# Kernel optimization log

Hardware: AMD Instinct MI355X
Metric: run time of the kernel (lower is better)

The kernel has to match this reference:

```python
import jax, jax.numpy as jnp
import numpy as np


def setup_inputs() -> dict:
    key = jax.random.key(0)
    ks = jax.random.split(key, 6)
    T, O, D = 1024, 512, 256
    H = 2 * D
    s = 1.0 / np.sqrt(H)
    return {
        "z_t": jax.random.normal(ks[0], (T, D), jnp.float32),
        "z_o": jax.random.normal(ks[1], (O, D), jnp.float32),
        "W1": jax.random.normal(ks[2], (H, H), jnp.float32) * s,
        "b1": jax.random.normal(ks[3], (H,), jnp.float32) * s,
        "W2": jax.random.normal(ks[4], (H, 1), jnp.float32) * s,
        "b2": jax.random.normal(ks[5], (1,), jnp.float32) * s,
    }


def reference(z_t, z_o, W1, b1, W2, b2):
    # Original: cat([z_t expand, z_o expand], -1) @ W1 + b1 -> LeakyReLU -> @ W2 + b2
    # Decompose the concat GEMM: [z_t | z_o] @ W1 == z_t @ W1[:D] + z_o @ W1[D:]
    D = z_t.shape[-1]
    ht = z_t @ W1[:D]              # [T, 2D]
    ho = z_o @ W1[D:]              # [O, 2D]
    h = ht[:, None, :] + ho[None, :, :] + b1   # [T, O, 2D]
    h = jax.nn.leaky_relu(h, negative_slope=0.01)
    out = jnp.squeeze(h @ W2, -1) + b2[0]      # [T, O]
    return out
```

## Files before the change

### kernel.cpp

```cpp
#include <hip/hip_runtime.h>
#include <cstdint>

#define T_DIM 1024
#define O_DIM 512
#define D_DIM 256
#define H_DIM 512
#define H2_DIM 256

typedef _Float16 f16x2 __attribute__((ext_vector_type(2)));
typedef _Float16 f16x8 __attribute__((ext_vector_type(8)));
typedef float f32x4 __attribute__((ext_vector_type(4)));

__device__ __forceinline__ uint32_t pack2(float a, float b) {
    f16x2 p;
    p.x = (_Float16)a;
    p.y = (_Float16)b;
    return __builtin_bit_cast(uint32_t, p);
}

__device__ __forceinline__ uint32_t pk_add(uint32_t a, uint32_t b) {
    uint32_t d;
    asm("v_pk_add_f16 %0, %1, %2" : "=v"(d) : "v"(a), "v"(b));
    return d;
}
__device__ __forceinline__ uint32_t pk_mul(uint32_t a, uint32_t b) {
    uint32_t d;
    asm("v_pk_mul_f16 %0, %1, %2" : "=v"(d) : "v"(a), "v"(b));
    return d;
}
__device__ __forceinline__ uint32_t pk_max(uint32_t a, uint32_t b) {
    uint32_t d;
    asm("v_pk_max_f16 %0, %1, %2" : "=v"(d) : "v"(a), "v"(b));
    return d;
}
__device__ __forceinline__ float dot2(uint32_t a, uint32_t b, float c) {
    float d;
    asm("v_dot2_f32_f16 %0, %1, %2, %3" : "=v"(d) : "v"(a), "v"(b), "v"(c));
    return d;
}

struct u4 { uint32_t x, y, z, w; };

#define GA_PAD 20

__global__ __launch_bounds__(256) void gemm_a(
    const float* __restrict__ z_t, const float* __restrict__ z_o,
    const float* __restrict__ W1, const float* __restrict__ b1,
    uint32_t* __restrict__ htT2, uint32_t* __restrict__ hoT2)
{
    const int bm = blockIdx.x;
    const int bn = blockIdx.y;
    const bool is_o = bm >= (T_DIM / 64);
    const float* Amat = is_o ? z_o : z_t;
    const int m0 = (is_o ? bm - T_DIM / 64 : bm) * 64;
    const int n0 = bn * 64;
    const int krow0 = is_o ? D_DIM : 0;
    const int Mdim = is_o ? O_DIM : T_DIM;
    uint32_t* outT2 = is_o ? hoT2 : htT2;

    __shared__ __align__(16) uint32_t lds_a[64 * GA_PAD];
    __shared__ __align__(16) uint32_t lds_w[64 * GA_PAD];

    const int tid = threadIdx.x;
    const int lane = tid & 63;
    const int wv = tid >> 6;
    const int quad = lane >> 4;
    const int l15 = lane & 15;

    f32x4 acc[4];
#pragma unroll
    for (int i = 0; i < 4; ++i) acc[i] = (f32x4)(0.0f);

    const int a_m = tid >> 2;
    const int a_kq = (tid & 3) * 8;
    const int w_kp = tid >> 4;
    const int w_nq = (tid & 15) * 4;

    for (int k0 = 0; k0 < D_DIM; k0 += 32) {
        {
            const float* p = &Amat[(size_t)(m0 + a_m) * D_DIM + k0 + a_kq];
            float4 v0 = *reinterpret_cast<const float4*>(p);
            float4 v1 = *reinterpret_cast<const float4*>(p + 4);
            lds_a[a_m * GA_PAD + a_kq / 2 + 0] = pack2(v0.x, v0.y);
            lds_a[a_m * GA_PAD + a_kq / 2 + 1] = pack2(v0.z, v0.w);
            lds_a[a_m * GA_PAD + a_kq / 2 + 2] = pack2(v1.x, v1.y);
            lds_a[a_m * GA_PAD + a_kq / 2 + 3] = pack2(v1.z, v1.w);
        }
        {
            const float* r0 = &W1[(size_t)(krow0 + k0 + 2 * w_kp) * H_DIM + n0 + w_nq];
            float4 a0 = *reinterpret_cast<const float4*>(r0);
            float4 a1 = *reinterpret_cast<const float4*>(r0 + H_DIM);
            lds_w[(w_nq + 0) * GA_PAD + w_kp] = pack2(a0.x, a1.x);
            lds_w[(w_nq + 1) * GA_PAD + w_kp] = pack2(a0.y, a1.y);
            lds_w[(w_nq + 2) * GA_PAD + w_kp] = pack2(a0.z, a1.z);
            lds_w[(w_nq + 3) * GA_PAD + w_kp] = pack2(a0.w, a1.w);
        }
        __syncthreads();

        u4 au;
        {
            const uint32_t* s = &lds_w[(wv * 16 + l15) * GA_PAD + quad * 4];
            au.x = s[0]; au.y = s[1]; au.z = s[2]; au.w = s[3];
        }
        f16x8 afrag = __builtin_bit_cast(f16x8, au);
#pragma unroll
        for (int mi = 0; mi < 4; ++mi) {
            u4 bu;
            const uint32_t* s = &lds_a[(mi * 16 + l15) * GA_PAD + quad * 4];
            bu.x = s[0]; bu.y = s[1]; bu.z = s[2]; bu.w = s[3];
            f16x8 bfrag = __builtin_bit_cast(f16x8, bu);
            acc[mi] = __builtin_amdgcn_mfma_f32_16x16x32_f16(afrag, bfrag,
                                                             acc[mi], 0, 0, 0);
        }
        __syncthreads();
    }

    const int nbase = n0 + wv * 16 + quad * 4;
    float b0 = 0.f, b1v = 0.f, b2v = 0.f, b3v = 0.f;
    if (!is_o) {
        b0 = b1[nbase + 0]; b1v = b1[nbase + 1];
        b2v = b1[nbase + 2]; b3v = b1[nbase + 3];
    }
#pragma unroll
    for (int mi = 0; mi < 4; ++mi) {
        const int m = m0 + mi * 16 + l15;
        outT2[(size_t)((nbase >> 1) + 0) * Mdim + m] = pack2(acc[mi][0] + b0, acc[mi][1] + b1v);
        outT2[(size_t)((nbase >> 1) + 1) * Mdim + m] = pack2(acc[mi][2] + b2v, acc[mi][3] + b3v);
    }
}

#define R_HC 64

__global__ __launch_bounds__(256) void reduce_b(
    const uint32_t* __restrict__ htT2, const uint32_t* __restrict__ hoT2,
    const float* __restrict__ W2, float* __restrict__ part)
{
    __shared__ __align__(16) uint32_t ht_s[R_HC * 64];
    __shared__ __align__(16) uint32_t ho_s[R_HC * 64];
    __shared__ uint32_t w2s[R_HC];

    const int tid = threadIdx.x;
    const int t0 = blockIdx.x * 64;
    const int o0 = blockIdx.y * 64;
    const int h2b = blockIdx.z * R_HC;

    if (tid < R_HC)
        w2s[tid] = pack2(W2[(h2b + tid) * 2], W2[(h2b + tid) * 2 + 1]);

#pragma unroll
    for (int r = 0; r < 4; ++r) {
        const int c = tid + r * 256;
        const int row = c >> 4;
        const int c4 = (c & 15) * 4;
        *reinterpret_cast<uint4*>(&ht_s[row * 64 + c4]) =
            *reinterpret_cast<const uint4*>(&htT2[(size_t)(h2b + row) * T_DIM + t0 + c4]);
        *reinterpret_cast<uint4*>(&ho_s[row * 64 + c4]) =
            *reinterpret_cast<const uint4*>(&hoT2[(size_t)(h2b + row) * O_DIM + o0 + c4]);
    }
    __syncthreads();

    const int tx = tid & 15;
    const int ty = tid >> 4;

    const uint32_t c001 = pack2(0.01f, 0.01f);

    float acc[4][4] = {};

#pragma unroll 4
    for (int h2 = 0; h2 < R_HC; ++h2) {
        const uint32_t w = w2s[h2];
        uint4 a = *reinterpret_cast<const uint4*>(&ht_s[h2 * 64 + ty * 4]);
        uint4 b = *reinterpret_cast<const uint4*>(&ho_s[h2 * 64 + tx * 4]);
        uint32_t av[4] = {a.x, a.y, a.z, a.w};
        uint32_t bv[4] = {b.x, b.y, b.z, b.w};
#pragma unroll
        for (int i = 0; i < 4; ++i)
#pragma unroll
            for (int j = 0; j < 4; ++j) {
                uint32_t s  = pk_add(av[i], bv[j]);
                uint32_t s2 = pk_mul(s, c001);
                uint32_t l  = pk_max(s, s2);
                acc[i][j]   = dot2(l, w, acc[i][j]);
            }
    }

    float* p = part + (size_t)blockIdx.z * T_DIM * O_DIM;
#pragma unroll
    for (int i = 0; i < 4; ++i) {
        float4 v = make_float4(acc[i][0], acc[i][1], acc[i][2], acc[i][3]);
        *reinterpret_cast<float4*>(
            &p[(size_t)(t0 + ty * 4 + i) * O_DIM + o0 + tx * 4]) = v;
    }
}

__global__ __launch_bounds__(256) void combine(
    const float* __restrict__ part, const float* __restrict__ b2,
    float* __restrict__ out)
{
    const float bb = b2[0];
    const int Q = T_DIM * O_DIM / 4;
#pragma unroll
    for (int r = 0; r < 2; ++r) {
        const int idx = blockIdx.x * 512 + r * 256 + threadIdx.x;
        const float4* p = reinterpret_cast<const float4*>(part);
        float4 s0 = p[idx];
        float4 s1 = p[idx + Q];
        float4 s2 = p[idx + 2 * Q];
        float4 s3 = p[idx + 3 * Q];
        float4 o;
        o.x = bb + (s0.x + s1.x) + (s2.x + s3.x);
        o.y = bb + (s0.y + s1.y) + (s2.y + s3.y);
        o.z = bb + (s0.z + s1.z) + (s2.z + s3.z);
        o.w = bb + (s0.w + s1.w) + (s2.w + s3.w);
        reinterpret_cast<float4*>(out)[idx] = o;
    }
}

extern "C" void kernel_launch(void* const* d_in, const int* in_sizes, int n_in,
                              void* d_out, int out_size, void* d_ws, size_t ws_size,
                              hipStream_t stream) {
    const float* z_t = (const float*)d_in[0];
    const float* z_o = (const float*)d_in[1];
    const float* W1  = (const float*)d_in[2];
    const float* b1  = (const float*)d_in[3];
    const float* W2  = (const float*)d_in[4];
    const float* b2  = (const float*)d_in[5];
    float* out = (float*)d_out;

    char* wsb = (char*)d_ws;
    uint32_t* htT2 = (uint32_t*)(wsb);
    uint32_t* hoT2 = (uint32_t*)(wsb + (1u << 20));
    float* part    = (float*)(wsb + 0x200000);

    dim3 gridA((T_DIM + O_DIM) / 64, H_DIM / 64);
    gemm_a<<<gridA, 256, 0, stream>>>(z_t, z_o, W1, b1, htT2, hoT2);

    dim3 gridB(T_DIM / 64, O_DIM / 64, H2_DIM / R_HC);
    reduce_b<<<gridB, 256, 0, stream>>>(htT2, hoT2, W2, part);

    combine<<<T_DIM * O_DIM / (4 * 512), 256, 0, stream>>>(part, b2, out);
}
```

Baseline: 95.54 us.

## Rewrite LeakyReLU as linear plus abs term, enlarge reduce tile, prefetch GEMM loads

The reduce kernel now uses the identity leaky_relu(x) = 0.505x + 0.495|x|. The inner loop computes only the abs term with a sign-bit mask, which replaces the multiply and max per element. The linear part is separable and is computed as per-row and per-column dot products with W2, then added back in combine. The reduce tile grows to 128x64 with 8x4 accumulators per thread and a software-prefetched next h2 row. The GEMM stage register-prefetches the next K slice of global loads so they overlap the MFMA work. The costs are higher register pressure, extra small workspace buffers and more reads in combine.

```diff
diff --git a/kernel.cpp b/kernel.cpp
--- a/kernel.cpp
+++ b/kernel.cpp
@@ -21,16 +21,6 @@
 __device__ __forceinline__ uint32_t pk_add(uint32_t a, uint32_t b) {
     uint32_t d;
     asm("v_pk_add_f16 %0, %1, %2" : "=v"(d) : "v"(a), "v"(b));
-    return d;
-}
-__device__ __forceinline__ uint32_t pk_mul(uint32_t a, uint32_t b) {
-    uint32_t d;
-    asm("v_pk_mul_f16 %0, %1, %2" : "=v"(d) : "v"(a), "v"(b));
-    return d;
-}
-__device__ __forceinline__ uint32_t pk_max(uint32_t a, uint32_t b) {
-    uint32_t d;
-    asm("v_pk_max_f16 %0, %1, %2" : "=v"(d) : "v"(a), "v"(b));
     return d;
 }
 __device__ __forceinline__ float dot2(uint32_t a, uint32_t b, float c) {
@@ -76,26 +66,36 @@
     const int w_kp = tid >> 4;
     const int w_nq = (tid & 15) * 4;
 
+    float4 va0, va1, wa0, wa1;
+    {
+        const float* p = &Amat[(size_t)(m0 + a_m) * D_DIM + a_kq];
+        va0 = *reinterpret_cast<const float4*>(p);
+        va1 = *reinterpret_cast<const float4*>(p + 4);
+        const float* r0 = &W1[(size_t)(krow0 + 2 * w_kp) * H_DIM + n0 + w_nq];
+        wa0 = *reinterpret_cast<const float4*>(r0);
+        wa1 = *reinterpret_cast<const float4*>(r0 + H_DIM);
+    }
+
     for (int k0 = 0; k0 < D_DIM; k0 += 32) {
-        {
-            const float* p = &Amat[(size_t)(m0 + a_m) * D_DIM + k0 + a_kq];
-            float4 v0 = *reinterpret_cast<const float4*>(p);
-            float4 v1 = *reinterpret_cast<const float4*>(p + 4);
-            lds_a[a_m * GA_PAD + a_kq / 2 + 0] = pack2(v0.x, v0.y);
-            lds_a[a_m * GA_PAD + a_kq / 2 + 1] = pack2(v0.z, v0.w);
-            lds_a[a_m * GA_PAD + a_kq / 2 + 2] = pack2(v1.x, v1.y);
-            lds_a[a_m * GA_PAD + a_kq / 2 + 3] = pack2(v1.z, v1.w);
+        lds_a[a_m * GA_PAD + a_kq / 2 + 0] = pack2(va0.x, va0.y);
+        lds_a[a_m * GA_PAD + a_kq / 2 + 1] = pack2(va0.z, va0.w);
+        lds_a[a_m * GA_PAD + a_kq / 2 + 2] = pack2(va1.x, va1.y);
+        lds_a[a_m * GA_PAD + a_kq / 2 + 3] = pack2(va1.z, va1.w);
+        lds_w[(w_nq + 0) * GA_PAD + w_kp] = pack2(wa0.x, wa1.x);
+        lds_w[(w_nq + 1) * GA_PAD + w_kp] = pack2(wa0.y, wa1.y);
+        lds_w[(w_nq + 2) * GA_PAD + w_kp] = pack2(wa0.z, wa1.z);
+        lds_w[(w_nq + 3) * GA_PAD + w_kp] = pack2(wa0.w, wa1.w);
+        __syncthreads();
+
+        if (k0 + 32 < D_DIM) {
+            const float* p = &Amat[(size_t)(m0 + a_m) * D_DIM + k0 + 32 + a_kq];
+            va0 = *reinterpret_cast<const float4*>(p);
+            va1 = *reinterpret_cast<const float4*>(p + 4);
+            const float* r0 =
+                &W1[(size_t)(krow0 + k0 + 32 + 2 * w_kp) * H_DIM + n0 + w_nq];
+            wa0 = *reinterpret_cast<const float4*>(r0);
+            wa1 = *reinterpret_cast<const float4*>(r0 + H_DIM);
         }
-        {
-            const float* r0 = &W1[(size_t)(krow0 + k0 + 2 * w_kp) * H_DIM + n0 + w_nq];
-            float4 a0 = *reinterpret_cast<const float4*>(r0);
-            float4 a1 = *reinterpret_cast<const float4*>(r0 + H_DIM);
-            lds_w[(w_nq + 0) * GA_PAD + w_kp] = pack2(a0.x, a1.x);
-            lds_w[(w_nq + 1) * GA_PAD + w_kp] = pack2(a0.y, a1.y);
-            lds_w[(w_nq + 2) * GA_PAD + w_kp] = pack2(a0.z, a1.z);
-            lds_w[(w_nq + 3) * GA_PAD + w_kp] = pack2(a0.w, a1.w);
-        }
-        __syncthreads();
 
         u4 au;
         {
@@ -129,89 +129,148 @@
     }
 }
 
-#define R_HC 64
+#define RB_T 128
+#define RB_O 64
+#define RB_H2 64
 
 __global__ __launch_bounds__(256) void reduce_b(
     const uint32_t* __restrict__ htT2, const uint32_t* __restrict__ hoT2,
-    const float* __restrict__ W2, float* __restrict__ part)
+    const float* __restrict__ W2, float* __restrict__ part,
+    float* __restrict__ ctp, float* __restrict__ cop)
 {
-    __shared__ __align__(16) uint32_t ht_s[R_HC * 64];
-    __shared__ __align__(16) uint32_t ho_s[R_HC * 64];
-    __shared__ uint32_t w2s[R_HC];
+    __shared__ __align__(16) uint32_t ht_s[RB_H2 * RB_T];
+    __shared__ __align__(16) uint32_t ho_s[RB_H2 * RB_O];
+    __shared__ uint32_t w2s[RB_H2];
+    __shared__ float red_t[2][RB_T];
+    __shared__ float red_o[4][RB_O];
 
     const int tid = threadIdx.x;
-    const int t0 = blockIdx.x * 64;
-    const int o0 = blockIdx.y * 64;
-    const int h2b = blockIdx.z * R_HC;
-
-    if (tid < R_HC)
-        w2s[tid] = pack2(W2[(h2b + tid) * 2], W2[(h2b + tid) * 2 + 1]);
-
+    const int t0 = blockIdx.x * RB_T;
+    const int o0 = blockIdx.y * RB_O;
+    const int h2b = blockIdx.z * RB_H2;
+
+    if (tid < RB_H2)
+        w2s[tid] = pack2(0.495f * W2[(h2b + tid) * 2],
+                         0.495f * W2[(h2b + tid) * 2 + 1]);
+
+#pragma unroll
+    for (int r = 0; r < 8; ++r) {
+        const int c = tid + r * 256;
+        const int row = c >> 5;
+        const int c4 = (c & 31) * 4;
+        *reinterpret_cast<uint4*>(&ht_s[row * RB_T + c4]) =
+            *reinterpret_cast<const uint4*>(
+                &htT2[(size_t)(h2b + row) * T_DIM + t0 + c4]);
+    }
 #pragma unroll
     for (int r = 0; r < 4; ++r) {
         const int c = tid + r * 256;
         const int row = c >> 4;
         const int c4 = (c & 15) * 4;
-        *reinterpret_cast<uint4*>(&ht_s[row * 64 + c4]) =
-            *reinterpret_cast<const uint4*>(&htT2[(size_t)(h2b + row) * T_DIM + t0 + c4]);
-        *reinterpret_cast<uint4*>(&ho_s[row * 64 + c4]) =
-            *reinterpret_cast<const uint4*>(&hoT2[(size_t)(h2b + row) * O_DIM + o0 + c4]);
+        *reinterpret_cast<uint4*>(&ho_s[row * RB_O + c4]) =
+            *reinterpret_cast<const uint4*>(
+                &hoT2[(size_t)(h2b + row) * O_DIM + o0 + c4]);
     }
     __syncthreads();
 
-    const int tx = tid & 15;
-    const int ty = tid >> 4;
-
-    const uint32_t c001 = pack2(0.01f, 0.01f);
-
-    float acc[4][4] = {};
+    const int og = tid & 15;
+    const int tg = tid >> 4;
+
+    float acc[8][4] = {};
+
+    uint4 a0 = *reinterpret_cast<const uint4*>(&ht_s[tg * 8]);
+    uint4 a1 = *reinterpret_cast<const uint4*>(&ht_s[tg * 8 + 4]);
+    uint4 b  = *reinterpret_cast<const uint4*>(&ho_s[og * 4]);
+    uint32_t w = w2s[0];
 
 #pragma unroll 4
-    for (int h2 = 0; h2 < R_HC; ++h2) {
-        const uint32_t w = w2s[h2];
-        uint4 a = *reinterpret_cast<const uint4*>(&ht_s[h2 * 64 + ty * 4]);
-        uint4 b = *reinterpret_cast<const uint4*>(&ho_s[h2 * 64 + tx * 4]);
-        uint32_t av[4] = {a.x, a.y, a.z, a.w};
-        uint32_t bv[4] = {b.x, b.y, b.z, b.w};
-#pragma unroll
-        for (int i = 0; i < 4; ++i)
+    for (int h2 = 0; h2 < RB_H2; ++h2) {
+        const int hn = (h2 + 1) & (RB_H2 - 1);
+        uint4 na0 = *reinterpret_cast<const uint4*>(&ht_s[hn * RB_T + tg * 8]);
+        uint4 na1 = *reinterpret_cast<const uint4*>(&ht_s[hn * RB_T + tg * 8 + 4]);
+        uint4 nb  = *reinterpret_cast<const uint4*>(&ho_s[hn * RB_O + og * 4]);
+        const uint32_t nw = w2s[hn];
+
+        const uint32_t av[8] = {a0.x, a0.y, a0.z, a0.w, a1.x, a1.y, a1.z, a1.w};
+        const uint32_t bv[4] = {b.x, b.y, b.z, b.w};
+#pragma unroll
+        for (int i = 0; i < 8; ++i)
 #pragma unroll
             for (int j = 0; j < 4; ++j) {
-                uint32_t s  = pk_add(av[i], bv[j]);
-                uint32_t s2 = pk_mul(s, c001);
-                uint32_t l  = pk_max(s, s2);
-                acc[i][j]   = dot2(l, w, acc[i][j]);
+                const uint32_t s = pk_add(av[i], bv[j]);
+                const uint32_t l = s & 0x7FFF7FFFu;
+                acc[i][j] = dot2(l, w, acc[i][j]);
             }
+        a0 = na0; a1 = na1; b = nb; w = nw;
     }
 
     float* p = part + (size_t)blockIdx.z * T_DIM * O_DIM;
 #pragma unroll
-    for (int i = 0; i < 4; ++i) {
+    for (int i = 0; i < 8; ++i) {
         float4 v = make_float4(acc[i][0], acc[i][1], acc[i][2], acc[i][3]);
         *reinterpret_cast<float4*>(
-            &p[(size_t)(t0 + ty * 4 + i) * O_DIM + o0 + tx * 4]) = v;
+            &p[(size_t)(t0 + tg * 8 + i) * O_DIM + o0 + og * 4]) = v;
+    }
+
+    {
+        const int t = tid & 127, half = tid >> 7;
+        float s = 0.f;
+#pragma unroll 8
+        for (int j = 0; j < 32; ++j)
+            s = dot2(ht_s[(half * 32 + j) * RB_T + t], w2s[half * 32 + j], s);
+        red_t[half][t] = s;
+        const int o = tid & 63, q = tid >> 6;
+        float so = 0.f;
+#pragma unroll 8
+        for (int j = 0; j < 16; ++j)
+            so = dot2(ho_s[(q * 16 + j) * RB_O + o], w2s[q * 16 + j], so);
+        red_o[q][o] = so;
+    }
+    __syncthreads();
+    if (tid < RB_T) {
+        ctp[(size_t)blockIdx.z * T_DIM + t0 + tid] = red_t[0][tid] + red_t[1][tid];
+    } else if (tid < RB_T + RB_O) {
+        const int o = tid - RB_T;
+        cop[(size_t)blockIdx.z * O_DIM + o0 + o] =
+            red_o[0][o] + red_o[1][o] + red_o[2][o] + red_o[3][o];
     }
 }
 
 __global__ __launch_bounds__(256) void combine(
-    const float* __restrict__ part, const float* __restrict__ b2,
+    const float* __restrict__ part, const float* __restrict__ ctp,
+    const float* __restrict__ cop, const float* __restrict__ b2,
     float* __restrict__ out)
 {
     const float bb = b2[0];
+    const float KLIN = 0.505f / 0.495f;
     const int Q = T_DIM * O_DIM / 4;
+    const float4* cop4 = reinterpret_cast<const float4*>(cop);
+    const float4* p4 = reinterpret_cast<const float4*>(part);
 #pragma unroll
     for (int r = 0; r < 2; ++r) {
         const int idx = blockIdx.x * 512 + r * 256 + threadIdx.x;
-        const float4* p = reinterpret_cast<const float4*>(part);
-        float4 s0 = p[idx];
-        float4 s1 = p[idx + Q];
-        float4 s2 = p[idx + 2 * Q];
-        float4 s3 = p[idx + 3 * Q];
+        const int t = idx >> 7;
+        const int oc = idx & 127;
+        const float ct = ctp[t] + ctp[T_DIM + t] + ctp[2 * T_DIM + t]
+                       + ctp[3 * T_DIM + t];
+        float4 co = cop4[oc];
+        const float4 c1 = cop4[128 + oc];
+        const float4 c2 = cop4[256 + oc];
+        const float4 c3 = cop4[384 + oc];
+        co.x += c1.x + c2.x + c3.x;
+        co.y += c1.y + c2.y + c3.y;
+        co.z += c1.z + c2.z + c3.z;
+        co.w += c1.w + c2.w + c3.w;
+        const float4 s0 = p4[idx];
+        const float4 s1 = p4[idx + Q];
+        const float4 s2 = p4[idx + 2 * Q];
+        const float4 s3 = p4[idx + 3 * Q];
+        const float base = bb + KLIN * ct;
         float4 o;
-        o.x = bb + (s0.x + s1.x) + (s2.x + s3.x);
-        o.y = bb + (s0.y + s1.y) + (s2.y + s3.y);
-        o.z = bb + (s0.z + s1.z) + (s2.z + s3.z);
-        o.w = bb + (s0.w + s1.w) + (s2.w + s3.w);
+        o.x = base + KLIN * co.x + (s0.x + s1.x) + (s2.x + s3.x);
+        o.y = base + KLIN * co.y + (s0.y + s1.y) + (s2.y + s3.y);
+        o.z = base + KLIN * co.z + (s0.z + s1.z) + (s2.z + s3.z);
+        o.w = base + KLIN * co.w + (s0.w + s1.w) + (s2.w + s3.w);
         reinterpret_cast<float4*>(out)[idx] = o;
     }
 }
@@ -229,14 +288,16 @@
 
     char* wsb = (char*)d_ws;
     uint32_t* htT2 = (uint32_t*)(wsb);
-    uint32_t* hoT2 = (uint32_t*)(wsb + (1u << 20));
+    uint32_t* hoT2 = (uint32_t*)(wsb + 0x100000);
+    float* ctp     = (float*)(wsb + 0x180000);
+    float* cop     = (float*)(wsb + 0x184000);
     float* part    = (float*)(wsb + 0x200000);
 
     dim3 gridA((T_DIM + O_DIM) / 64, H_DIM / 64);
     gemm_a<<<gridA, 256, 0, stream>>>(z_t, z_o, W1, b1, htT2, hoT2);
 
-    dim3 gridB(T_DIM / 64, O_DIM / 64, H2_DIM / R_HC);
-    reduce_b<<<gridB, 256, 0, stream>>>(htT2, hoT2, W2, part);
-
-    combine<<<T_DIM * O_DIM / (4 * 512), 256, 0, stream>>>(part, b2, out);
-}
+    dim3 gridB(T_DIM / RB_T, O_DIM / RB_O, H2_DIM / RB_H2);
+    reduce_b<<<gridB, 256, 0, stream>>>(htT2, hoT2, W2, part, ctp, cop);
+
+    combine<<<T_DIM * O_DIM / (4 * 512), 256, 0, stream>>>(part, ctp, cop, b2, out);
+}
```

Result: no change. 94.62 us (-1.0%).
